# Performance work log

Hardware: AMD Instinct MI355X
Metric: run time of the kernel (lower is better)

The kernel has to match this reference:

```python
import jax, jax.numpy as jnp
import numpy as np

HEADS = 4
NEG = -1e30


def layer_norm(x, g, b, eps=1e-5):
    m = x.mean(-1, keepdims=True)
    v = ((x - m) ** 2).mean(-1, keepdims=True)
    return (x - m) / jnp.sqrt(v + eps) * g + b


def setup_inputs() -> dict:
    key = jax.random.key(0)
    B, S, H, V, L = 16, 512, 1024, 8000, 8
    ks = jax.random.split(key, 12)
    inp = {}
    inp['x'] = jax.random.randint(ks[0], (B, S), 0, V)
    inp['lengths'] = jax.random.randint(ks[1], (B,), 4, S + 1)
    inp['emb'] = jax.random.normal(ks[2], (V, H), jnp.float32) * 0.02
    inp['Wq'] = jax.random.normal(ks[3], (L, H, H), jnp.float32) * 0.02
    inp['bq'] = jnp.zeros((L, H), jnp.float32)
    inp['Wk'] = jax.random.normal(ks[4], (L, H, H), jnp.float32) * 0.02
    inp['bk'] = jnp.zeros((L, H), jnp.float32)
    inp['Wv'] = jax.random.normal(ks[5], (L, H, H), jnp.float32) * 0.02
    inp['bv'] = jnp.zeros((L, H), jnp.float32)
    inp['W1'] = jax.random.normal(ks[6], (L, H, H), jnp.float32) * 0.02
    inp['b1'] = jnp.zeros((L, H), jnp.float32)
    inp['W2'] = jax.random.normal(ks[7], (L, H, H), jnp.float32) * 0.02
    inp['b2'] = jnp.zeros((L, H), jnp.float32)
    inp['g1'] = jnp.ones((L, H), jnp.float32)
    inp['be1'] = jnp.zeros((L, H), jnp.float32)
    inp['g2'] = jnp.ones((L, H), jnp.float32)
    inp['be2'] = jnp.zeros((L, H), jnp.float32)
    inp['Wfc'] = jax.random.normal(ks[8], (H, H), jnp.float32) * 0.02
    inp['bfc'] = jnp.zeros((H,), jnp.float32)
    return inp


def reference(x, lengths, emb, Wq, bq, Wk, bk, Wv, bv, W1, b1, W2, b2, g1, be1, g2, be2, Wfc, bfc):
    B, S = x.shape
    V, H = emb.shape
    dh = H // HEADS
    L = Wq.shape[0]
    # token embedding + sinusoidal positional encoding
    pos = jnp.arange(S, dtype=jnp.float32)[:, None]
    div = jnp.exp(jnp.arange(0, H, 2, dtype=jnp.float32) * (-np.log(10000.0) / H))
    pe = jnp.zeros((S, H), jnp.float32)
    pe = pe.at[:, 0::2].set(jnp.sin(pos * div)).at[:, 1::2].set(jnp.cos(pos * div))
    z = emb[x] + pe[None]
    # masks: causal + padding on queries + (faithful source quirk) head index < length
    i = jnp.arange(S)
    causal = i[None, :] <= i[:, None]                                   # [S,S]
    q_valid = i[None, :] < lengths[:, None]                             # [B,S]
    h_valid = jnp.arange(HEADS)[None, :] < lengths[:, None]             # [B,HEADS]
    row_valid = q_valid[:, None, :, None] & h_valid[:, :, None, None]   # [B,HEADS,S,1]
    mask = causal[None, None] & row_valid                               # [B,HEADS,S,S]
    scale = 1.0 / np.sqrt(H)  # faithful: scales by sqrt(HIDDEN), not head dim
    atten_last = None
    for l in range(L):
        q = (z @ Wq[l].T + bq[l]).reshape(B, S, HEADS, dh).transpose(0, 2, 1, 3)
        k = (z @ Wk[l].T + bk[l]).reshape(B, S, HEADS, dh).transpose(0, 2, 1, 3)
        v = (z @ Wv[l].T + bv[l]).reshape(B, S, HEADS, dh).transpose(0, 2, 1, 3)
        s = jnp.einsum('bhqd,bhkd->bhqk', q, k) * scale
        p = jax.nn.softmax(jnp.where(mask, s, NEG), axis=-1)
        p = jnp.where(row_valid, p, 0.0)  # zero fully-masked rows (source's atten>0 trick)
        o = jnp.einsum('bhqk,bhkd->bhqd', p, v)
        # faithful source bug: reshape [B,HEADS,S,dh] -> [B,S,H] WITHOUT transposing heads back
        o = o.reshape(B, S, H)
        atten_last = p.max(axis=-1)  # [B,HEADS,S]
        z1 = layer_norm(z + o, g1[l], be1[l])
        f = jax.nn.gelu(z1 @ W1[l].T + b1[l], approximate=False) @ W2[l].T + b2[l]
        z = layer_norm(z1 + f, g2[l], be2[l])
    out_fc = z @ Wfc.T + bfc
    logits = out_fc @ emb.T  # tied output projection
    y_prim = jax.nn.softmax(logits, axis=-1)
    return y_prim, atten_last
```

## Files before the change

kernel.cpp:

```cpp
#include <hip/hip_runtime.h>
#include <math.h>


typedef unsigned short u16;
typedef unsigned int u32;
typedef __attribute__((ext_vector_type(8))) short short8;
typedef __attribute__((ext_vector_type(4))) float f32x4;

__device__ __forceinline__ u16 f2bf(float f) {
    u32 u = __builtin_bit_cast(u32, f);
    u32 r = (u + 0x7FFFu + ((u >> 16) & 1u)) >> 16;
    return (u16)r;
}
__device__ __forceinline__ float bf2f(u16 u) {
    u32 v = ((u32)u) << 16;
    return __builtin_bit_cast(float, v);
}
__device__ __forceinline__ float4 unpack4(uint2 r) {
    float4 f;
    f.x = __builtin_bit_cast(float, r.x << 16);
    f.y = __builtin_bit_cast(float, r.x & 0xffff0000u);
    f.z = __builtin_bit_cast(float, r.y << 16);
    f.w = __builtin_bit_cast(float, r.y & 0xffff0000u);
    return f;
}

__device__ __forceinline__ void stage16(const void* g, void* ldsbase, int lane) {
#if __has_builtin(__builtin_amdgcn_global_load_lds)
    __builtin_amdgcn_global_load_lds(
        (const __attribute__((address_space(1))) u32*)g,
        (__attribute__((address_space(3))) u32*)ldsbase, 16, 0, 0);
#else
    *(short8*)((u16*)ldsbase + lane * 8) = *(const short8*)g;
#endif
}

__global__ __launch_bounds__(256, 2) void gemm_p(
    const u16* __restrict__ A, const u16* __restrict__ B,
    const float* __restrict__ bias, void* __restrict__ C,
    int M, int N, int K, int ldc, int Nstore, int flags,
    u16* __restrict__ VtOut)
{
    __shared__ u16 As[2][128 * 64];
    __shared__ u16 Bs[2][128 * 64];
    const int tid = threadIdx.x;
    const int w = tid >> 6, lane = tid & 63;
    const int nwg = gridDim.x * gridDim.y;
    int bid = blockIdx.y * gridDim.x + blockIdx.x;
    if ((nwg & 7) == 0) bid = (bid & 7) * (nwg >> 3) + (bid >> 3);
    const int n0 = (bid % gridDim.x) * 128;
    const int m0 = (bid / gridDim.x) * 128;

    const int lr = lane >> 3;
    const int lc = lane & 7;

    auto stages = [&](int buf, int kt) {
        const int k0 = kt * 64;
#pragma unroll
        for (int i = 0; i < 4; ++i) {
            const int ra = (w * 4 + i) * 8 + lr;
            const int ca = lc ^ (ra & 7);
            stage16(A + (size_t)(m0 + ra) * K + k0 + ca * 8,
                    &As[buf][(w * 4 + i) * 512], lane);
            stage16(B + (size_t)(n0 + ra) * K + k0 + ca * 8,
                    &Bs[buf][(w * 4 + i) * 512], lane);
        }
    };

    f32x4 acc[4][4];
#pragma unroll
    for (int i = 0; i < 4; ++i)
#pragma unroll
        for (int j = 0; j < 4; ++j) {
            acc[i][j][0] = 0.f; acc[i][j][1] = 0.f;
            acc[i][j][2] = 0.f; acc[i][j][3] = 0.f;
        }
    const int row = lane & 15, quad = lane >> 4;
    const int wm = (w >> 1) * 64, wn = (w & 1) * 64;
    const int nt = K >> 6;

    stages(0, 0);
    if (nt > 1) stages(1, 1);

    for (int t = 0; t < nt; ++t) {
        if (t + 1 < nt) asm volatile("s_waitcnt vmcnt(8)" ::: "memory");
        else            asm volatile("s_waitcnt vmcnt(0)" ::: "memory");
        __builtin_amdgcn_s_barrier();
        __builtin_amdgcn_sched_barrier(0);
        const int buf = t & 1;
#pragma unroll
        for (int kk = 0; kk < 2; ++kk) {
            const int g0 = kk * 4 + quad;
            short8 af[4], bfr[4];
#pragma unroll
            for (int i = 0; i < 4; ++i) {
                const int r = wm + i * 16 + row;
                af[i] = *(const short8*)&As[buf][r * 64 + ((g0 ^ (r & 7)) * 8)];
            }
#pragma unroll
            for (int j = 0; j < 4; ++j) {
                const int r = wn + j * 16 + row;
                bfr[j] = *(const short8*)&Bs[buf][r * 64 + ((g0 ^ (r & 7)) * 8)];
            }
            __builtin_amdgcn_s_setprio(1);
#pragma unroll
            for (int i = 0; i < 4; ++i)
#pragma unroll
                for (int j = 0; j < 4; ++j)
                    acc[i][j] = __builtin_amdgcn_mfma_f32_16x16x32_bf16(
                        af[i], bfr[j], acc[i][j], 0, 0, 0);
            __builtin_amdgcn_s_setprio(0);
        }
        __builtin_amdgcn_sched_barrier(0);
        __builtin_amdgcn_s_barrier();
        if (t + 2 < nt) stages(buf, t + 2);
    }

    const int do_bf = flags & 1, do_gelu = flags & 2, do_qkv = flags & 4;
#pragma unroll
    for (int i = 0; i < 4; ++i)
#pragma unroll
        for (int j = 0; j < 4; ++j) {
            const int gr0 = m0 + wm + i * 16 + quad * 4;
            const int gc = n0 + wn + j * 16 + row;
            if (gc < Nstore) {
                const float bv = bias ? bias[gc] : 0.f;
                if (do_qkv && gc >= 2048) {
                    const int d = gc - 2048;
                    const int bb = gr0 >> 9, s = gr0 & 511;
                    ushort4 ov;
                    ov.x = f2bf(acc[i][j][0] + bv);
                    ov.y = f2bf(acc[i][j][1] + bv);
                    ov.z = f2bf(acc[i][j][2] + bv);
                    ov.w = f2bf(acc[i][j][3] + bv);
                    *(ushort4*)(VtOut +
                        (((size_t)(bb * 4 + (d >> 8)) * 256 + (d & 255)) * 512 + s)) = ov;
                } else {
#pragma unroll
                    for (int r = 0; r < 4; ++r) {
                        float v = acc[i][j][r] + bv;
                        if (do_gelu) v = 0.5f * v * (1.f + erff(v * 0.7071067811865475f));
                        if (do_bf) ((u16*)C)[(size_t)(gr0 + r) * ldc + gc] = f2bf(v);
                        else       ((float*)C)[(size_t)(gr0 + r) * ldc + gc] = v;
                    }
                }
            }
        }
}

__global__ __launch_bounds__(256, 2) void attn_mfma(
    const u16* __restrict__ QK, const u16* __restrict__ Vt,
    const int* __restrict__ lengths,
    float* __restrict__ O, float* __restrict__ atten)
{
    __shared__ u16 sK[64 * 256];
    __shared__ u16 sV[256 * 64];
    __shared__ u16 sP[4][16 * 64];
    const int qt = blockIdx.x, h = blockIdx.y, b = blockIdx.z;
    const int q0 = qt * 64;
    const int t = threadIdx.x;
    const int w = t >> 6, lane = t & 63;
    const int row = lane & 15, quad = lane >> 4;

    {
        const u16* qbase = QK + (size_t)(b * 512 + q0) * 2048 + h * 256;
        const int r2 = lane >> 5, c = lane & 31;
#pragma unroll
        for (int i = 0; i < 8; ++i) {
            const int rr = w * 16 + i * 2 + r2;
            stage16(qbase + (size_t)rr * 2048 + ((c ^ (rr & 7)) * 8),
                    &sK[(w * 16 + i * 2) * 256], lane);
        }
    }
    __syncthreads();
    short8 qf[8];
    {
        const int qr = w * 16 + row;
#pragma unroll
        for (int ds = 0; ds < 8; ++ds) {
            const int chunk = ds * 4 + quad;
            qf[ds] = *(const short8*)&sK[qr * 256 + ((chunk ^ (qr & 7)) * 8)];
        }
    }
    __syncthreads();

    float mrow[4], lrow[4];
#pragma unroll
    for (int j = 0; j < 4; ++j) { mrow[j] = -3.0e38f; lrow[j] = 0.f; }
    f32x4 oacc[16];
#pragma unroll
    for (int dt = 0; dt < 16; ++dt) {
        oacc[dt][0] = 0.f; oacc[dt][1] = 0.f; oacc[dt][2] = 0.f; oacc[dt][3] = 0.f;
    }

    const int nkt = qt + 1;
    for (int kt = 0; kt < nkt; ++kt) {
        const int k0 = kt * 64;
        {
            const u16* kbase = QK + (size_t)(b * 512 + k0) * 2048 + 1024 + h * 256;
            const int r2 = lane >> 5, c = lane & 31;
#pragma unroll
            for (int i = 0; i < 8; ++i) {
                const int rr = w * 16 + i * 2 + r2;
                stage16(kbase + (size_t)rr * 2048 + ((c ^ (rr & 7)) * 8),
                        &sK[(w * 16 + i * 2) * 256], lane);
            }
            const u16* vbase = Vt + ((size_t)(b * 4 + h) * 256) * 512 + k0;
            const int vr = lane >> 3, vc = lane & 7;
#pragma unroll
            for (int i = 0; i < 8; ++i) {
                const int dd = w * 64 + i * 8 + vr;
                stage16(vbase + (size_t)dd * 512 + ((vc ^ (dd & 7)) * 8),
                        &sV[(w * 64 + i * 8) * 64], lane);
            }
        }
        __syncthreads();

        f32x4 sacc[4];
#pragma unroll
        for (int kt4 = 0; kt4 < 4; ++kt4) {
            sacc[kt4][0] = 0.f; sacc[kt4][1] = 0.f;
            sacc[kt4][2] = 0.f; sacc[kt4][3] = 0.f;
        }
#pragma unroll
        for (int ds = 0; ds < 8; ++ds) {
            const int chunk = ds * 4 + quad;
#pragma unroll
            for (int kt4 = 0; kt4 < 4; ++kt4) {
                const int kr = kt4 * 16 + row;
                const short8 kf = *(const short8*)&sK[kr * 256 + ((chunk ^ (kr & 7)) * 8)];
                sacc[kt4] = __builtin_amdgcn_mfma_f32_16x16x32_bf16(
                    qf[ds], kf, sacc[kt4], 0, 0, 0);
            }
        }

        const int diag = (kt == qt);
        float sc[4][4];
#pragma unroll
        for (int kt4 = 0; kt4 < 4; ++kt4)
#pragma unroll
            for (int j = 0; j < 4; ++j) {
                float v = sacc[kt4][j] * 0.03125f;
                if (diag && (kt4 * 16 + row > w * 16 + quad * 4 + j)) v = -3.0e38f;
                sc[kt4][j] = v;
            }
        float alpha[4];
#pragma unroll
        for (int j = 0; j < 4; ++j) {
            float lm = fmaxf(fmaxf(sc[0][j], sc[1][j]), fmaxf(sc[2][j], sc[3][j]));
            lm = fmaxf(lm, __shfl_xor(lm, 1));
            lm = fmaxf(lm, __shfl_xor(lm, 2));
            lm = fmaxf(lm, __shfl_xor(lm, 4));
            lm = fmaxf(lm, __shfl_xor(lm, 8));
            const float mnew = fmaxf(mrow[j], lm);
            alpha[j] = __expf(mrow[j] - mnew);
            float ps = 0.f;
#pragma unroll
            for (int kt4 = 0; kt4 < 4; ++kt4) {
                sc[kt4][j] = __expf(sc[kt4][j] - mnew);
                ps += sc[kt4][j];
            }
            ps += __shfl_xor(ps, 1);
            ps += __shfl_xor(ps, 2);
            ps += __shfl_xor(ps, 4);
            ps += __shfl_xor(ps, 8);
            lrow[j] = lrow[j] * alpha[j] + ps;
            mrow[j] = mnew;
        }
#pragma unroll
        for (int kt4 = 0; kt4 < 4; ++kt4)
#pragma unroll
            for (int j = 0; j < 4; ++j) {
                const int ql = quad * 4 + j;
                const int k = kt4 * 16 + row;
                sP[w][ql * 64 + (((k >> 3) ^ (ql & 7)) * 8) + (k & 7)] = f2bf(sc[kt4][j]);
            }
#pragma unroll
        for (int dt = 0; dt < 16; ++dt) {
            oacc[dt][0] *= alpha[0]; oacc[dt][1] *= alpha[1];
            oacc[dt][2] *= alpha[2]; oacc[dt][3] *= alpha[3];
        }
#pragma unroll
        for (int kk = 0; kk < 2; ++kk) {
            const int chunk = kk * 4 + quad;
            const short8 pf = *(const short8*)&sP[w][row * 64 + ((chunk ^ (row & 7)) * 8)];
#pragma unroll
            for (int dt = 0; dt < 16; ++dt) {
                const int dr = dt * 16 + row;
                const short8 vf = *(const short8*)&sV[dr * 64 + ((chunk ^ (dr & 7)) * 8)];
                oacc[dt] = __builtin_amdgcn_mfma_f32_16x16x32_bf16(
                    pf, vf, oacc[dt], 0, 0, 0);
            }
        }
        __syncthreads();
    }

    const int len = lengths[b];
#pragma unroll
    for (int j = 0; j < 4; ++j) {
        const int qg = q0 + w * 16 + quad * 4 + j;
        const float linv = (qg < len) ? 1.f / lrow[j] : 0.f;
        float* op = O + ((size_t)((b * 4 + h) * 512 + qg)) * 256;
#pragma unroll
        for (int dt = 0; dt < 16; ++dt)
            op[dt * 16 + row] = oacc[dt][j] * linv;
        if (atten && row == 0)
            atten[(size_t)(b * 4 + h) * 512 + qg] = linv;
    }
}

__global__ __launch_bounds__(256) void embed_kernel(
    const int* __restrict__ x, const float* __restrict__ emb,
    float* __restrict__ Z, u16* __restrict__ Zb)
{
    const int tokidx = blockIdx.x;
    const int s = tokidx & 511;
    const int t = threadIdx.x;
    const int tok = x[tokidx];
    const int c0 = t << 2;
    float4 e = *(const float4*)(emb + (size_t)tok * 1024 + c0);
    float pe[4];
#pragma unroll
    for (int j = 0; j < 4; ++j) {
        int c = c0 + j;
        float freq = expf((float)(c & ~1) * (-9.210340371976184f / 1024.f));
        float arg = (float)s * freq;
        pe[j] = (c & 1) ? cosf(arg) : sinf(arg);
    }
    float4 o = make_float4(e.x + pe[0], e.y + pe[1], e.z + pe[2], e.w + pe[3]);
    *(float4*)(Z + (size_t)tokidx * 1024 + c0) = o;
    ushort4 ob = {f2bf(o.x), f2bf(o.y), f2bf(o.z), f2bf(o.w)};
    ((ushort4*)(Zb + (size_t)tokidx * 1024))[t] = ob;
}

__global__ __launch_bounds__(256) void add_ln(
    const float* __restrict__ X, const float* __restrict__ R,
    const float* __restrict__ g, const float* __restrict__ be,
    float* __restrict__ Y, u16* __restrict__ Yb)
{
    __shared__ float red[8];
    const int row = blockIdx.x;
    const int t = threadIdx.x;
    const float4 x = ((const float4*)(X + (size_t)row * 1024))[t];
    const float4 r = ((const float4*)(R + (size_t)row * 1024))[t];
    float v[4] = {x.x + r.x, x.y + r.y, x.z + r.z, x.w + r.w};
    float s = v[0] + v[1] + v[2] + v[3];
#pragma unroll
    for (int off = 32; off; off >>= 1) s += __shfl_xor(s, off);
    const int wid = t >> 6;
    if ((t & 63) == 0) red[wid] = s;
    __syncthreads();
    s = red[0] + red[1] + red[2] + red[3];
    const float mean = s * (1.f / 1024.f);
    float q = 0.f;
#pragma unroll
    for (int j = 0; j < 4; ++j) { float d = v[j] - mean; q += d * d; }
#pragma unroll
    for (int off = 32; off; off >>= 1) q += __shfl_xor(q, off);
    if ((t & 63) == 0) red[4 + wid] = q;
    __syncthreads();
    q = red[4] + red[5] + red[6] + red[7];
    const float rstd = rsqrtf(q * (1.f / 1024.f) + 1e-5f);
    const float4 gv = ((const float4*)g)[t];
    const float4 bv = ((const float4*)be)[t];
    float4 o;
    o.x = (v[0] - mean) * rstd * gv.x + bv.x;
    o.y = (v[1] - mean) * rstd * gv.y + bv.y;
    o.z = (v[2] - mean) * rstd * gv.z + bv.z;
    o.w = (v[3] - mean) * rstd * gv.w + bv.w;
    ((float4*)(Y + (size_t)row * 1024))[t] = o;
    ushort4 ob = {f2bf(o.x), f2bf(o.y), f2bf(o.z), f2bf(o.w)};
    ((ushort4*)(Yb + (size_t)row * 1024))[t] = ob;
}

__global__ __launch_bounds__(256) void softmax8000(float* __restrict__ P)
{
    __shared__ float red[8];
    float* p = P + (size_t)blockIdx.x * 8000;
    const int t = threadIdx.x;
    float vals[32];
    float mx = -3.0e38f;
#pragma unroll
    for (int j = 0; j < 32; ++j) {
        int c = t + (j << 8);
        if (c < 8000) { vals[j] = p[c]; mx = fmaxf(mx, vals[j]); }
    }
#pragma unroll
    for (int off = 32; off; off >>= 1) mx = fmaxf(mx, __shfl_xor(mx, off));
    const int wid = t >> 6;
    if ((t & 63) == 0) red[wid] = mx;
    __syncthreads();
    mx = fmaxf(fmaxf(red[0], red[1]), fmaxf(red[2], red[3]));
    float sum = 0.f;
#pragma unroll
    for (int j = 0; j < 32; ++j) {
        int c = t + (j << 8);
        if (c < 8000) { vals[j] = expf(vals[j] - mx); sum += vals[j]; }
    }
#pragma unroll
    for (int off = 32; off; off >>= 1) sum += __shfl_xor(sum, off);
    if ((t & 63) == 0) red[4 + wid] = sum;
    __syncthreads();
    const float inv = 1.f / (red[4] + red[5] + red[6] + red[7]);
#pragma unroll
    for (int j = 0; j < 32; ++j) {
        int c = t + (j << 8);
        if (c < 8000) p[c] = vals[j] * inv;
    }
}

__global__ __launch_bounds__(256) void cvt_qkv(
    const float* __restrict__ Wq, const float* __restrict__ Wk,
    const float* __restrict__ Wv, u16* __restrict__ dst)
{
    const int n = blockIdx.x, l = blockIdx.y, t = threadIdx.x;
    const float* src = (n < 1024) ? Wq + ((size_t)l * 1024 + n) * 1024
                     : (n < 2048) ? Wk + ((size_t)l * 1024 + (n - 1024)) * 1024
                                  : Wv + ((size_t)l * 1024 + (n - 2048)) * 1024;
    float4 v = ((const float4*)src)[t];
    ushort4 o = {f2bf(v.x), f2bf(v.y), f2bf(v.z), f2bf(v.w)};
    ((ushort4*)(dst + ((size_t)l * 3072 + n) * 1024))[t] = o;
}

__global__ __launch_bounds__(256) void cvt_bias_qkv(
    const float* __restrict__ bq, const float* __restrict__ bk,
    const float* __restrict__ bv, float* __restrict__ dst)
{
    const int i = blockIdx.x * 256 + threadIdx.x;
    if (i >= 8 * 3072) return;
    const int l = i / 3072, n = i - l * 3072;
    float v = (n < 1024) ? bq[l * 1024 + n]
            : (n < 2048) ? bk[l * 1024 + (n - 1024)]
                         : bv[l * 1024 + (n - 2048)];
    dst[i] = v;
}

__global__ __launch_bounds__(256) void cvt_plain(
    const float* __restrict__ src, u16* __restrict__ dst, int n)
{
    const int i = (blockIdx.x * 256 + threadIdx.x) * 4;
    if (i >= n) return;
    float4 v = *(const float4*)(src + i);
    ushort4 o = {f2bf(v.x), f2bf(v.y), f2bf(v.z), f2bf(v.w)};
    *(ushort4*)(dst + i) = o;
}

__global__ __launch_bounds__(256) void cvt_emb(
    const float* __restrict__ emb, u16* __restrict__ dst)
{
    const int r = blockIdx.x, t = threadIdx.x;
    ushort4 o = {0, 0, 0, 0};
    if (r < 8000) {
        float4 v = ((const float4*)(emb + (size_t)r * 1024))[t];
        o.x = f2bf(v.x); o.y = f2bf(v.y); o.z = f2bf(v.z); o.w = f2bf(v.w);
    }
    ((ushort4*)(dst + (size_t)r * 1024))[t] = o;
}

extern "C" void kernel_launch(void* const* d_in, const int* in_sizes, int n_in,
                              void* d_out, int out_size, void* d_ws, size_t ws_size,
                              hipStream_t stream)
{
    (void)in_sizes; (void)n_in; (void)out_size;
    const int*   x       = (const int*)d_in[0];
    const int*   lengths = (const int*)d_in[1];
    const float* emb = (const float*)d_in[2];
    const float* Wq  = (const float*)d_in[3];
    const float* bq  = (const float*)d_in[4];
    const float* Wk  = (const float*)d_in[5];
    const float* bk  = (const float*)d_in[6];
    const float* Wv  = (const float*)d_in[7];
    const float* bv  = (const float*)d_in[8];
    const float* W1  = (const float*)d_in[9];
    const float* b1  = (const float*)d_in[10];
    const float* W2  = (const float*)d_in[11];
    const float* b2  = (const float*)d_in[12];
    const float* g1  = (const float*)d_in[13];
    const float* be1 = (const float*)d_in[14];
    const float* g2  = (const float*)d_in[15];
    const float* be2 = (const float*)d_in[16];
    const float* Wfc = (const float*)d_in[17];
    const float* bfc = (const float*)d_in[18];

    float* out = (float*)d_out;
    float* atten = out + (size_t)65536000;

    const size_t SZ_EMBB = (size_t)8064 * 1024 * 2;
    const size_t SZ_FCB  = (size_t)8192 * 1024 * 2;
    const size_t SZ_BQKV = (size_t)8 * 3072 * 4;
    const size_t SZ_WQKV = (size_t)8 * 3072 * 1024 * 2;
    const size_t SZ_W12  = (size_t)8 * 1024 * 1024 * 2;
    const size_t SZ_WFC  = (size_t)1024 * 1024 * 2;
    const size_t SZ_Z    = (size_t)8192 * 1024 * 4;
    const size_t SZ_ZB   = (size_t)8192 * 1024 * 2;
    const size_t SZ_QKB  = (size_t)8192 * 2048 * 2;
    const size_t SZ_VT   = (size_t)16 * 4 * 256 * 512 * 2;
    const size_t NONFORCED = SZ_WQKV + 2 * SZ_W12 + SZ_WFC + 2 * SZ_Z + SZ_ZB
                           + SZ_QKB + SZ_VT + SZ_Z;
    const size_t FORCED = SZ_EMBB + SZ_FCB + SZ_BQKV;
    const size_t GRAND = FORCED + NONFORCED;

    char* wsc = (char*)d_ws;
    char* oc  = (char*)d_out;
    const size_t ocap = (size_t)65536000 * 4;
    size_t wo = 0, oo = 0;
    const bool all_ws = ws_size >= GRAND;
    u16*   emb_bf = (u16*)(wsc + wo);  wo += SZ_EMBB;
    u16*   fc_b   = (u16*)(wsc + wo);  wo += SZ_FCB;
    float* bqkv   = (float*)(wsc + wo); wo += SZ_BQKV;
    auto alloc = [&](size_t sz) -> char* {
        if (all_ws) { char* p = wsc + wo; wo += sz; return p; }
        if (oo + sz <= ocap) { char* p = oc + oo; oo += sz; return p; }
        char* p = wsc + wo; wo += sz; return p;
    };
    u16*   Wqkv_bf = (u16*)alloc(SZ_WQKV);
    u16*   W1b     = (u16*)alloc(SZ_W12);
    u16*   W2b     = (u16*)alloc(SZ_W12);
    u16*   Wfcb    = (u16*)alloc(SZ_WFC);
    float* z       = (float*)alloc(SZ_Z);
    float* z1      = (float*)alloc(SZ_Z);
    u16*   zb      = (u16*)alloc(SZ_ZB);
    u16*   qkb     = (u16*)alloc(SZ_QKB);
    u16*   vtb     = (u16*)alloc(SZ_VT);
    float* o       = (float*)alloc(SZ_Z);
    u16* z1b = qkb;
    u16* f1b = qkb + (size_t)8192 * 1024;

    dim3 blk(256);
    cvt_qkv<<<dim3(3072, 8), blk, 0, stream>>>(Wq, Wk, Wv, Wqkv_bf);
    cvt_bias_qkv<<<96, blk, 0, stream>>>(bq, bk, bv, bqkv);
    cvt_plain<<<8192, blk, 0, stream>>>(W1, W1b, 8 * 1024 * 1024);
    cvt_plain<<<8192, blk, 0, stream>>>(W2, W2b, 8 * 1024 * 1024);
    cvt_plain<<<1024, blk, 0, stream>>>(Wfc, Wfcb, 1024 * 1024);
    cvt_emb<<<8064, blk, 0, stream>>>(emb, emb_bf);

    embed_kernel<<<8192, blk, 0, stream>>>(x, emb, z, zb);

    for (int l = 0; l < 8; ++l) {
        const size_t WO1 = (size_t)l * 1024 * 1024;
        const size_t BO = (size_t)l * 1024;
        gemm_p<<<dim3(24, 64), blk, 0, stream>>>(
            zb, Wqkv_bf + (size_t)l * 3072 * 1024, bqkv + (size_t)l * 3072,
            qkb, 8192, 3072, 1024, 2048, 3072, 1 | 4, vtb);
        attn_mfma<<<dim3(8, 4, 16), blk, 0, stream>>>(
            qkb, vtb, lengths, o, (l == 7) ? atten : nullptr);
        add_ln<<<8192, blk, 0, stream>>>(z, o, g1 + BO, be1 + BO, z1, z1b);
        gemm_p<<<dim3(8, 64), blk, 0, stream>>>(
            z1b, W1b + WO1, b1 + BO, f1b, 8192, 1024, 1024, 1024, 1024, 1 | 2, nullptr);
        gemm_p<<<dim3(8, 64), blk, 0, stream>>>(
            f1b, W2b + WO1, b2 + BO, o, 8192, 1024, 1024, 1024, 1024, 0, nullptr);
        add_ln<<<8192, blk, 0, stream>>>(z1, o, g2 + BO, be2 + BO, z, zb);
    }
    gemm_p<<<dim3(8, 64), blk, 0, stream>>>(
        zb, Wfcb, bfc, fc_b, 8192, 1024, 1024, 1024, 1024, 1, nullptr);
    gemm_p<<<dim3(63, 64), blk, 0, stream>>>(
        fc_b, emb_bf, nullptr, out, 8192, 8064, 1024, 8000, 8000, 0, nullptr);
    softmax8000<<<8192, blk, 0, stream>>>(out);
}
```

Before: 2.759 ms.

## Use 256x256 GEMM tiles with 8 waves and 4-stage LDS pipeline

Replaces the 128x128, 4-wave GEMM with a 256x256 tile computed by 8 waves (each 128x64), using K-steps of 32 and a 4-slot LDS ring buffer with three tiles prefetched ahead. The larger tile raises arithmetic intensity and cuts global traffic, and the deeper prefetch hides load latency. Costs are more registers per thread (32 accumulator tiles), 64KB of LDS per block, fewer blocks (384 for QKV, 128 for FFN) on a large-CU device, and padding the embedding table to 8192 rows for the vocabulary GEMM.

```diff
diff --git a/kernel.cpp b/kernel.cpp
--- a/kernel.cpp
+++ b/kernel.cpp
@@ -35,110 +35,111 @@
 #endif
 }
 
-__global__ __launch_bounds__(256, 2) void gemm_p(
+__global__ __launch_bounds__(512, 2) void gemm_8p(
     const u16* __restrict__ A, const u16* __restrict__ B,
     const float* __restrict__ bias, void* __restrict__ C,
     int M, int N, int K, int ldc, int Nstore, int flags,
     u16* __restrict__ VtOut)
 {
-    __shared__ u16 As[2][128 * 64];
-    __shared__ u16 Bs[2][128 * 64];
+    __shared__ u16 As[4][128 * 64];
+    __shared__ u16 Bs[4][128 * 64];
     const int tid = threadIdx.x;
     const int w = tid >> 6, lane = tid & 63;
     const int nwg = gridDim.x * gridDim.y;
     int bid = blockIdx.y * gridDim.x + blockIdx.x;
     if ((nwg & 7) == 0) bid = (bid & 7) * (nwg >> 3) + (bid >> 3);
-    const int n0 = (bid % gridDim.x) * 128;
-    const int m0 = (bid / gridDim.x) * 128;
-
-    const int lr = lane >> 3;
-    const int lc = lane & 7;
-
-    auto stages = [&](int buf, int kt) {
-        const int k0 = kt * 64;
-#pragma unroll
-        for (int i = 0; i < 4; ++i) {
-            const int ra = (w * 4 + i) * 8 + lr;
-            const int ca = lc ^ (ra & 7);
-            stage16(A + (size_t)(m0 + ra) * K + k0 + ca * 8,
-                    &As[buf][(w * 4 + i) * 512], lane);
-            stage16(B + (size_t)(n0 + ra) * K + k0 + ca * 8,
-                    &Bs[buf][(w * 4 + i) * 512], lane);
+    const int n0 = (bid % gridDim.x) * 256;
+    const int m0 = (bid / gridDim.x) * 256;
+
+    auto stageC = [&](int slot, int kt) {
+        const int k0 = kt * 32;
+#pragma unroll
+        for (int i = 0; i < 2; ++i) {
+            const int rq = (w * 2 + i) * 8 + (lane >> 3);
+            const int s  = (lane & 7) ^ (rq & 7);
+            const int gr = rq * 2 + (s >> 2);
+            const int gk = (s & 3) * 8;
+            stage16(A + (size_t)(m0 + gr) * K + k0 + gk,
+                    &As[slot][(w * 2 + i) * 512], lane);
+            stage16(B + (size_t)(n0 + gr) * K + k0 + gk,
+                    &Bs[slot][(w * 2 + i) * 512], lane);
         }
     };
 
-    f32x4 acc[4][4];
-#pragma unroll
-    for (int i = 0; i < 4; ++i)
+    f32x4 acc[8][4];
+#pragma unroll
+    for (int i = 0; i < 8; ++i)
 #pragma unroll
         for (int j = 0; j < 4; ++j) {
             acc[i][j][0] = 0.f; acc[i][j][1] = 0.f;
             acc[i][j][2] = 0.f; acc[i][j][3] = 0.f;
         }
-    const int row = lane & 15, quad = lane >> 4;
-    const int wm = (w >> 1) * 64, wn = (w & 1) * 64;
-    const int nt = K >> 6;
-
-    stages(0, 0);
-    if (nt > 1) stages(1, 1);
+    const int col = lane & 15, quad = lane >> 4;
+    const int wm = w >> 2, wn = w & 3;
+    const int nt = K >> 5;
+
+    stageC(0, 0); stageC(1, 1); stageC(2, 2);
 
     for (int t = 0; t < nt; ++t) {
-        if (t + 1 < nt) asm volatile("s_waitcnt vmcnt(8)" ::: "memory");
-        else            asm volatile("s_waitcnt vmcnt(0)" ::: "memory");
+        if (t + 3 < nt) stageC((t + 3) & 3, t + 3);
+        const int rem = nt - 1 - t;
+        if (rem >= 3)      asm volatile("s_waitcnt vmcnt(12)" ::: "memory");
+        else if (rem == 2) asm volatile("s_waitcnt vmcnt(8)" ::: "memory");
+        else if (rem == 1) asm volatile("s_waitcnt vmcnt(4)" ::: "memory");
+        else               asm volatile("s_waitcnt vmcnt(0)" ::: "memory");
         __builtin_amdgcn_s_barrier();
         __builtin_amdgcn_sched_barrier(0);
-        const int buf = t & 1;
-#pragma unroll
-        for (int kk = 0; kk < 2; ++kk) {
-            const int g0 = kk * 4 + quad;
-            short8 af[4], bfr[4];
-#pragma unroll
-            for (int i = 0; i < 4; ++i) {
-                const int r = wm + i * 16 + row;
-                af[i] = *(const short8*)&As[buf][r * 64 + ((g0 ^ (r & 7)) * 8)];
-            }
-#pragma unroll
-            for (int j = 0; j < 4; ++j) {
-                const int r = wn + j * 16 + row;
-                bfr[j] = *(const short8*)&Bs[buf][r * 64 + ((g0 ^ (r & 7)) * 8)];
-            }
-            __builtin_amdgcn_s_setprio(1);
-#pragma unroll
-            for (int i = 0; i < 4; ++i)
-#pragma unroll
-                for (int j = 0; j < 4; ++j)
-                    acc[i][j] = __builtin_amdgcn_mfma_f32_16x16x32_bf16(
-                        af[i], bfr[j], acc[i][j], 0, 0, 0);
-            __builtin_amdgcn_s_setprio(0);
-        }
+        const int sl = t & 3;
+        short8 af[8], bf4[4];
+#pragma unroll
+        for (int mf = 0; mf < 8; ++mf) {
+            const int gr = wm * 128 + mf * 16 + col;
+            const int rq = gr >> 1;
+            const int sp = (((gr & 1) << 2) | quad) ^ (rq & 7);
+            af[mf] = *(const short8*)&As[sl][rq * 64 + sp * 8];
+        }
+#pragma unroll
+        for (int nf = 0; nf < 4; ++nf) {
+            const int gr = wn * 64 + nf * 16 + col;
+            const int rq = gr >> 1;
+            const int sp = (((gr & 1) << 2) | quad) ^ (rq & 7);
+            bf4[nf] = *(const short8*)&Bs[sl][rq * 64 + sp * 8];
+        }
+        __builtin_amdgcn_s_setprio(1);
+#pragma unroll
+        for (int mf = 0; mf < 8; ++mf)
+#pragma unroll
+            for (int nf = 0; nf < 4; ++nf)
+                acc[mf][nf] = __builtin_amdgcn_mfma_f32_16x16x32_bf16(
+                    af[mf], bf4[nf], acc[mf][nf], 0, 0, 0);
+        __builtin_amdgcn_s_setprio(0);
         __builtin_amdgcn_sched_barrier(0);
         __builtin_amdgcn_s_barrier();
-        if (t + 2 < nt) stages(buf, t + 2);
     }
 
     const int do_bf = flags & 1, do_gelu = flags & 2, do_qkv = flags & 4;
 #pragma unroll
-    for (int i = 0; i < 4; ++i)
-#pragma unroll
-        for (int j = 0; j < 4; ++j) {
-            const int gr0 = m0 + wm + i * 16 + quad * 4;
-            const int gc = n0 + wn + j * 16 + row;
+    for (int mf = 0; mf < 8; ++mf)
+#pragma unroll
+        for (int nf = 0; nf < 4; ++nf) {
+            const int gr0 = m0 + wm * 128 + mf * 16 + quad * 4;
+            const int gc = n0 + wn * 64 + nf * 16 + col;
             if (gc < Nstore) {
                 const float bv = bias ? bias[gc] : 0.f;
                 if (do_qkv && gc >= 2048) {
                     const int d = gc - 2048;
                     const int bb = gr0 >> 9, s = gr0 & 511;
                     ushort4 ov;
-                    ov.x = f2bf(acc[i][j][0] + bv);
-                    ov.y = f2bf(acc[i][j][1] + bv);
-                    ov.z = f2bf(acc[i][j][2] + bv);
-                    ov.w = f2bf(acc[i][j][3] + bv);
+                    ov.x = f2bf(acc[mf][nf][0] + bv);
+                    ov.y = f2bf(acc[mf][nf][1] + bv);
+                    ov.z = f2bf(acc[mf][nf][2] + bv);
+                    ov.w = f2bf(acc[mf][nf][3] + bv);
                     *(ushort4*)(VtOut +
                         (((size_t)(bb * 4 + (d >> 8)) * 256 + (d & 255)) * 512 + s)) = ov;
                 } else {
 #pragma unroll
                     for (int r = 0; r < 4; ++r) {
-                        float v = acc[i][j][r] + bv;
+                        float v = acc[mf][nf][r] + bv;
                         if (do_gelu) v = 0.5f * v * (1.f + erff(v * 0.7071067811865475f));
                         if (do_bf) ((u16*)C)[(size_t)(gr0 + r) * ldc + gc] = f2bf(v);
                         else       ((float*)C)[(size_t)(gr0 + r) * ldc + gc] = v;
@@ -485,7 +486,7 @@
     float* out = (float*)d_out;
     float* atten = out + (size_t)65536000;
 
-    const size_t SZ_EMBB = (size_t)8064 * 1024 * 2;
+    const size_t SZ_EMBB = (size_t)8192 * 1024 * 2;
     const size_t SZ_FCB  = (size_t)8192 * 1024 * 2;
     const size_t SZ_BQKV = (size_t)8 * 3072 * 4;
     const size_t SZ_WQKV = (size_t)8 * 3072 * 1024 * 2;
@@ -526,34 +527,34 @@
     u16* z1b = qkb;
     u16* f1b = qkb + (size_t)8192 * 1024;
 
-    dim3 blk(256);
+    dim3 blk(256), blk8(512);
     cvt_qkv<<<dim3(3072, 8), blk, 0, stream>>>(Wq, Wk, Wv, Wqkv_bf);
     cvt_bias_qkv<<<96, blk, 0, stream>>>(bq, bk, bv, bqkv);
     cvt_plain<<<8192, blk, 0, stream>>>(W1, W1b, 8 * 1024 * 1024);
     cvt_plain<<<8192, blk, 0, stream>>>(W2, W2b, 8 * 1024 * 1024);
     cvt_plain<<<1024, blk, 0, stream>>>(Wfc, Wfcb, 1024 * 1024);
-    cvt_emb<<<8064, blk, 0, stream>>>(emb, emb_bf);
+    cvt_emb<<<8192, blk, 0, stream>>>(emb, emb_bf);
 
     embed_kernel<<<8192, blk, 0, stream>>>(x, emb, z, zb);
 
     for (int l = 0; l < 8; ++l) {
         const size_t WO1 = (size_t)l * 1024 * 1024;
         const size_t BO = (size_t)l * 1024;
-        gemm_p<<<dim3(24, 64), blk, 0, stream>>>(
+        gemm_8p<<<dim3(12, 32), blk8, 0, stream>>>(
             zb, Wqkv_bf + (size_t)l * 3072 * 1024, bqkv + (size_t)l * 3072,
             qkb, 8192, 3072, 1024, 2048, 3072, 1 | 4, vtb);
         attn_mfma<<<dim3(8, 4, 16), blk, 0, stream>>>(
             qkb, vtb, lengths, o, (l == 7) ? atten : nullptr);
         add_ln<<<8192, blk, 0, stream>>>(z, o, g1 + BO, be1 + BO, z1, z1b);
-        gemm_p<<<dim3(8, 64), blk, 0, stream>>>(
+        gemm_8p<<<dim3(4, 32), blk8, 0, stream>>>(
             z1b, W1b + WO1, b1 + BO, f1b, 8192, 1024, 1024, 1024, 1024, 1 | 2, nullptr);
-        gemm_p<<<dim3(8, 64), blk, 0, stream>>>(
+        gemm_8p<<<dim3(4, 32), blk8, 0, stream>>>(
             f1b, W2b + WO1, b2 + BO, o, 8192, 1024, 1024, 1024, 1024, 0, nullptr);
         add_ln<<<8192, blk, 0, stream>>>(z1, o, g2 + BO, be2 + BO, z, zb);
     }
-    gemm_p<<<dim3(8, 64), blk, 0, stream>>>(
+    gemm_8p<<<dim3(4, 32), blk8, 0, stream>>>(
         zb, Wfcb, bfc, fc_b, 8192, 1024, 1024, 1024, 1024, 1, nullptr);
-    gemm_p<<<dim3(63, 64), blk, 0, stream>>>(
-        fc_b, emb_bf, nullptr, out, 8192, 8064, 1024, 8000, 8000, 0, nullptr);
+    gemm_8p<<<dim3(32, 32), blk8, 0, stream>>>(
+        fc_b, emb_bf, nullptr, out, 8192, 8192, 1024, 8000, 8000, 0, nullptr);
     softmax8000<<<8192, blk, 0, stream>>>(out);
 }
```

Result: slower. 3.551 ms (+28.7%).
